# Performance work log

Hardware: AMD Instinct MI355X
Metric: run time of the kernel (lower is better)

## Reference

```python
import jax, jax.numpy as jnp
import numpy as np

TOP_K = 4
TAU = 1.0  # training-mode temperature
EPS_NORM = 1e-12
EPS_G = 1e-10


def l2_normalize(x, axis=-1):
    sq = jnp.sum(x * x, axis=axis, keepdims=True)
    return x * jax.lax.rsqrt(jnp.maximum(sq, EPS_NORM))


def setup_inputs() -> dict:
    key = jax.random.key(0)
    k1, k2, k3, k4 = jax.random.split(key, 4)
    B, S, D = 256, 196, 1024
    P, L = 512, 8
    x_embed = jax.random.normal(k1, (B, S, D), dtype=jnp.float32)
    prompt = jax.random.normal(k2, (P, L, D), dtype=jnp.float32) * 0.02
    prompt_key = jax.random.normal(k3, (P, D), dtype=jnp.float32) * 0.02
    gumbel_u = jax.random.uniform(k4, (TOP_K, B, P), dtype=jnp.float32)
    return {"x_embed": x_embed, "prompt": prompt, "prompt_key": prompt_key,
            "gumbel_u": gumbel_u}


def reference(x_embed, prompt, prompt_key, gumbel_u):
    # query: mean over sequence dim (embedding_key='mean')  -> [B, D]
    query = jnp.mean(x_embed, axis=1)
    key_n = l2_normalize(prompt_key, axis=1)   # [P, D]
    q_n = l2_normalize(query, axis=1)          # [B, D]
    sim = jnp.matmul(q_n, key_n.T)             # [B, P]

    P = prompt.shape[0]
    cur = sim
    selected = []
    for i in range(TOP_K):
        # Gumbel(0,1) noise from uniform samples
        g = -jnp.log(-jnp.log(gumbel_u[i] + EPS_G) + EPS_G)
        soft = jax.nn.softmax((cur + g) / TAU, axis=-1)      # [B, P]
        hard = jax.nn.one_hot(jnp.argmax(soft, axis=-1), P, dtype=soft.dtype)
        w = soft + jax.lax.stop_gradient(hard - soft)        # straight-through
        # weighted combination over pool -> [B, L, D]
        sel = jnp.einsum('bp,pld->bld', w, prompt)
        selected.append(sel)
        # training-mode mask-out of selected entries
        cur = cur - w * 1000.0
    return jnp.concatenate(selected, axis=1)  # [B, TOP_K*L, D]
```

## Files before the change

kernel.cpp:

```cpp
#include <hip/hip_runtime.h>
#include <hip/hip_bf16.h>
#include <math.h>

#define B   256
#define S   196
#define D   1024
#define P   512
#define L   8
#define TOPK 4

#define SSPLIT 7
#define SCHUNK (S / SSPLIT)
#define KSPLIT 8

__global__ __launch_bounds__(256) void mean_partial_kernel(
    const float* __restrict__ x, float* __restrict__ part) {
  const int b = blockIdx.x;
  const int j = blockIdx.y;
  const int t = threadIdx.x;
  const float* xb = x + (size_t)b * S * D + (size_t)j * SCHUNK * D + t * 4;

  float4 acc = make_float4(0.f, 0.f, 0.f, 0.f);
#pragma unroll 4
  for (int s = 0; s < SCHUNK; ++s) {
    float4 v = *(const float4*)(xb + (size_t)s * D);
    acc.x += v.x; acc.y += v.y; acc.z += v.z; acc.w += v.w;
  }
  *(float4*)(part + ((size_t)b * SSPLIT + j) * D + t * 4) = acc;
}

__global__ __launch_bounds__(256) void norm_kernel(
    const float* __restrict__ part, const float* __restrict__ pk,
    float* __restrict__ qn, float* __restrict__ kn) {
  const int t = threadIdx.x;
  float4 acc;
  float* dst;

  if (blockIdx.x < B) {
    const int b = blockIdx.x;
    acc = make_float4(0.f, 0.f, 0.f, 0.f);
#pragma unroll
    for (int j = 0; j < SSPLIT; ++j) {
      float4 v = *(const float4*)(part + ((size_t)b * SSPLIT + j) * D + t * 4);
      acc.x += v.x; acc.y += v.y; acc.z += v.z; acc.w += v.w;
    }
    const float inv = 1.0f / (float)S;
    acc.x *= inv; acc.y *= inv; acc.z *= inv; acc.w *= inv;
    dst = qn + (size_t)b * D + t * 4;
  } else {
    const int p = blockIdx.x - B;
    acc = *(const float4*)(pk + (size_t)p * D + t * 4);
    dst = kn + (size_t)p * D + t * 4;
  }

  float ss = acc.x * acc.x + acc.y * acc.y + acc.z * acc.z + acc.w * acc.w;
  for (int off = 32; off > 0; off >>= 1) ss += __shfl_down(ss, off, 64);
  __shared__ float wsum[4];
  __shared__ float snorm;
  const int lane = t & 63, w = t >> 6;
  if (lane == 0) wsum[w] = ss;
  __syncthreads();
  if (t == 0) {
    float tot = wsum[0] + wsum[1] + wsum[2] + wsum[3];
    snorm = rsqrtf(fmaxf(tot, 1e-12f));
  }
  __syncthreads();
  const float r = snorm;
  *(float4*)dst = make_float4(acc.x * r, acc.y * r, acc.z * r, acc.w * r);
}

#define KK 16
__global__ __launch_bounds__(256) void sim_kernel(
    const float* __restrict__ qn, const float* __restrict__ kn,
    float* __restrict__ simp) {
  const int b0 = blockIdx.x * 64;
  const int p0 = blockIdx.y * 64;
  const int z  = blockIdx.z;
  const int k0 = z * (D / KSPLIT);
  const int t = threadIdx.x;
  const int tx = t & 15;
  const int ty = t >> 4;

  __shared__ float As[KK][68];
  __shared__ float Bs[KK][68];

  float acc[4][4];
#pragma unroll
  for (int i = 0; i < 4; ++i)
#pragma unroll
    for (int j = 0; j < 4; ++j) acc[i][j] = 0.f;

  const int rr = t >> 2;
  const int k4 = (t & 3) * 4;

  for (int kt = 0; kt < D / KSPLIT; kt += KK) {
    float4 a = *(const float4*)(qn + (size_t)(b0 + rr) * D + k0 + kt + k4);
    float4 bb = *(const float4*)(kn + (size_t)(p0 + rr) * D + k0 + kt + k4);
    As[k4 + 0][rr] = a.x; As[k4 + 1][rr] = a.y;
    As[k4 + 2][rr] = a.z; As[k4 + 3][rr] = a.w;
    Bs[k4 + 0][rr] = bb.x; Bs[k4 + 1][rr] = bb.y;
    Bs[k4 + 2][rr] = bb.z; Bs[k4 + 3][rr] = bb.w;
    __syncthreads();
#pragma unroll
    for (int kk = 0; kk < KK; ++kk) {
      float4 av = *(const float4*)&As[kk][ty * 4];
      float4 bv = *(const float4*)&Bs[kk][tx * 4];
      acc[0][0] += av.x * bv.x; acc[0][1] += av.x * bv.y;
      acc[0][2] += av.x * bv.z; acc[0][3] += av.x * bv.w;
      acc[1][0] += av.y * bv.x; acc[1][1] += av.y * bv.y;
      acc[1][2] += av.y * bv.z; acc[1][3] += av.y * bv.w;
      acc[2][0] += av.z * bv.x; acc[2][1] += av.z * bv.y;
      acc[2][2] += av.z * bv.z; acc[2][3] += av.z * bv.w;
      acc[3][0] += av.w * bv.x; acc[3][1] += av.w * bv.y;
      acc[3][2] += av.w * bv.z; acc[3][3] += av.w * bv.w;
    }
    __syncthreads();
  }
#pragma unroll
  for (int i = 0; i < 4; ++i)
#pragma unroll
    for (int j = 0; j < 4; ++j)
      simp[((size_t)z * B + b0 + ty * 4 + i) * P + p0 + tx * 4 + j] =
          acc[i][j];
}

__global__ __launch_bounds__(256) void select_gather_kernel(
    const float* __restrict__ simp, const float* __restrict__ gu,
    const float* __restrict__ prompt, float* __restrict__ out) {
  const int b = blockIdx.x;
  const int t = threadIdx.x;
  __shared__ float cur[P];

  float c0 = 0.f, c1 = 0.f;
#pragma unroll
  for (int z = 0; z < KSPLIT; ++z) {
    c0 += simp[((size_t)z * B + b) * P + t];
    c1 += simp[((size_t)z * B + b) * P + t + 256];
  }
  cur[t] = c0;
  cur[t + 256] = c1;
  __syncthreads();

  __shared__ float wval[4];
  __shared__ int widx[4];
  __shared__ int sidx[TOPK];

  for (int i = 0; i < TOPK; ++i) {
    const float* gui = gu + ((size_t)i * B + b) * P;
    float u0 = gui[t];
    float u1 = gui[t + 256];
    float g0 = -logf(-logf(u0 + 1e-10f) + 1e-10f);
    float g1 = -logf(-logf(u1 + 1e-10f) + 1e-10f);
    float v0 = cur[t] + g0;
    float v1 = cur[t + 256] + g1;
    float bv = v0; int bi = t;
    if (v1 > bv) { bv = v1; bi = t + 256; }
    for (int off = 32; off > 0; off >>= 1) {
      float ov = __shfl_down(bv, off, 64);
      int oi = __shfl_down(bi, off, 64);
      if (ov > bv || (ov == bv && oi < bi)) { bv = ov; bi = oi; }
    }
    const int lane = t & 63, w = t >> 6;
    if (lane == 0) { wval[w] = bv; widx[w] = bi; }
    __syncthreads();
    if (t == 0) {
      float bestv = wval[0]; int besti = widx[0];
      for (int k = 1; k < 4; ++k)
        if (wval[k] > bestv || (wval[k] == bestv && widx[k] < besti)) {
          bestv = wval[k]; besti = widx[k];
        }
      sidx[i] = besti;
      cur[besti] -= 1000.0f;
    }
    __syncthreads();
  }

#pragma unroll
  for (int i = 0; i < TOPK; ++i) {
    const int p = sidx[i];
    const float4* src = (const float4*)(prompt + (size_t)p * L * D);
    float4* dst = (float4*)(out + ((size_t)b * (TOPK * L) + i * L) * D);
#pragma unroll
    for (int l = 0; l < L; ++l) {
      dst[l * (D / 4) + t] = src[l * (D / 4) + t];
    }
  }
}

extern "C" void kernel_launch(void* const* d_in, const int* in_sizes, int n_in,
                              void* d_out, int out_size, void* d_ws,
                              size_t ws_size, hipStream_t stream) {
  const float* x_embed    = (const float*)d_in[0];
  const float* prompt     = (const float*)d_in[1];
  const float* prompt_key = (const float*)d_in[2];
  const float* gumbel_u   = (const float*)d_in[3];
  float* out = (float*)d_out;

  float* simp = (float*)d_ws;
  float* qn   = simp + (size_t)KSPLIT * B * P;
  float* kn   = qn + (size_t)B * D;
  float* part = kn + (size_t)P * D;

  mean_partial_kernel<<<dim3(B, SSPLIT), 256, 0, stream>>>(x_embed, part);
  norm_kernel<<<B + P, 256, 0, stream>>>(part, prompt_key, qn, kn);
  sim_kernel<<<dim3(B / 64, P / 64, KSPLIT), 256, 0, stream>>>(qn, kn, simp);
  select_gather_kernel<<<B, 256, 0, stream>>>(simp, gumbel_u, prompt, out);
}
```

Measured before the change: 329.8 us.

## Fuse normalization, similarity and selection into one kernel using output as scratch

Removes the separate norm and split-K similarity GEMM kernels. Each batch block now computes its query mean and norm, then dots the query against all prompt keys while computing key norms on the fly, then does the Gumbel top-k selection and gather. Partial means are stored in the output buffer as scratch instead of a workspace. This cuts two launches and the intermediate global traffic, but every block redundantly rereads the full prompt_key matrix and recomputes key norms.

```diff
diff --git a/kernel.cpp b/kernel.cpp
--- a/kernel.cpp
+++ b/kernel.cpp
@@ -1,20 +1,19 @@
 #include <hip/hip_runtime.h>
-#include <hip/hip_bf16.h>
 #include <math.h>
 
-#define B   256
-#define S   196
-#define D   1024
-#define P   512
-#define L   8
+#define B    256
+#define S    196
+#define D    1024
+#define P    512
+#define L    8
 #define TOPK 4
 
 #define SSPLIT 7
 #define SCHUNK (S / SSPLIT)
-#define KSPLIT 8
+#define OUTSTRIDE (TOPK * L * D)
 
 __global__ __launch_bounds__(256) void mean_partial_kernel(
-    const float* __restrict__ x, float* __restrict__ part) {
+    const float* __restrict__ x, float* __restrict__ scratch) {
   const int b = blockIdx.x;
   const int j = blockIdx.y;
   const int t = threadIdx.x;
@@ -26,151 +25,99 @@
     float4 v = *(const float4*)(xb + (size_t)s * D);
     acc.x += v.x; acc.y += v.y; acc.z += v.z; acc.w += v.w;
   }
-  *(float4*)(part + ((size_t)b * SSPLIT + j) * D + t * 4) = acc;
+  *(float4*)(scratch + (size_t)b * OUTSTRIDE + j * D + t * 4) = acc;
 }
 
-__global__ __launch_bounds__(256) void norm_kernel(
-    const float* __restrict__ part, const float* __restrict__ pk,
-    float* __restrict__ qn, float* __restrict__ kn) {
-  const int t = threadIdx.x;
-  float4 acc;
-  float* dst;
-
-  if (blockIdx.x < B) {
-    const int b = blockIdx.x;
-    acc = make_float4(0.f, 0.f, 0.f, 0.f);
-#pragma unroll
-    for (int j = 0; j < SSPLIT; ++j) {
-      float4 v = *(const float4*)(part + ((size_t)b * SSPLIT + j) * D + t * 4);
-      acc.x += v.x; acc.y += v.y; acc.z += v.z; acc.w += v.w;
-    }
-    const float inv = 1.0f / (float)S;
-    acc.x *= inv; acc.y *= inv; acc.z *= inv; acc.w *= inv;
-    dst = qn + (size_t)b * D + t * 4;
-  } else {
-    const int p = blockIdx.x - B;
-    acc = *(const float4*)(pk + (size_t)p * D + t * 4);
-    dst = kn + (size_t)p * D + t * 4;
-  }
-
-  float ss = acc.x * acc.x + acc.y * acc.y + acc.z * acc.z + acc.w * acc.w;
-  for (int off = 32; off > 0; off >>= 1) ss += __shfl_down(ss, off, 64);
-  __shared__ float wsum[4];
-  __shared__ float snorm;
-  const int lane = t & 63, w = t >> 6;
-  if (lane == 0) wsum[w] = ss;
-  __syncthreads();
-  if (t == 0) {
-    float tot = wsum[0] + wsum[1] + wsum[2] + wsum[3];
-    snorm = rsqrtf(fmaxf(tot, 1e-12f));
-  }
-  __syncthreads();
-  const float r = snorm;
-  *(float4*)dst = make_float4(acc.x * r, acc.y * r, acc.z * r, acc.w * r);
-}
-
-#define KK 16
-__global__ __launch_bounds__(256) void sim_kernel(
-    const float* __restrict__ qn, const float* __restrict__ kn,
-    float* __restrict__ simp) {
-  const int b0 = blockIdx.x * 64;
-  const int p0 = blockIdx.y * 64;
-  const int z  = blockIdx.z;
-  const int k0 = z * (D / KSPLIT);
-  const int t = threadIdx.x;
-  const int tx = t & 15;
-  const int ty = t >> 4;
-
-  __shared__ float As[KK][68];
-  __shared__ float Bs[KK][68];
-
-  float acc[4][4];
-#pragma unroll
-  for (int i = 0; i < 4; ++i)
-#pragma unroll
-    for (int j = 0; j < 4; ++j) acc[i][j] = 0.f;
-
-  const int rr = t >> 2;
-  const int k4 = (t & 3) * 4;
-
-  for (int kt = 0; kt < D / KSPLIT; kt += KK) {
-    float4 a = *(const float4*)(qn + (size_t)(b0 + rr) * D + k0 + kt + k4);
-    float4 bb = *(const float4*)(kn + (size_t)(p0 + rr) * D + k0 + kt + k4);
-    As[k4 + 0][rr] = a.x; As[k4 + 1][rr] = a.y;
-    As[k4 + 2][rr] = a.z; As[k4 + 3][rr] = a.w;
-    Bs[k4 + 0][rr] = bb.x; Bs[k4 + 1][rr] = bb.y;
-    Bs[k4 + 2][rr] = bb.z; Bs[k4 + 3][rr] = bb.w;
-    __syncthreads();
-#pragma unroll
-    for (int kk = 0; kk < KK; ++kk) {
-      float4 av = *(const float4*)&As[kk][ty * 4];
-      float4 bv = *(const float4*)&Bs[kk][tx * 4];
-      acc[0][0] += av.x * bv.x; acc[0][1] += av.x * bv.y;
-      acc[0][2] += av.x * bv.z; acc[0][3] += av.x * bv.w;
-      acc[1][0] += av.y * bv.x; acc[1][1] += av.y * bv.y;
-      acc[1][2] += av.y * bv.z; acc[1][3] += av.y * bv.w;
-      acc[2][0] += av.z * bv.x; acc[2][1] += av.z * bv.y;
-      acc[2][2] += av.z * bv.z; acc[2][3] += av.z * bv.w;
-      acc[3][0] += av.w * bv.x; acc[3][1] += av.w * bv.y;
-      acc[3][2] += av.w * bv.z; acc[3][3] += av.w * bv.w;
-    }
-    __syncthreads();
-  }
-#pragma unroll
-  for (int i = 0; i < 4; ++i)
-#pragma unroll
-    for (int j = 0; j < 4; ++j)
-      simp[((size_t)z * B + b0 + ty * 4 + i) * P + p0 + tx * 4 + j] =
-          acc[i][j];
-}
-
-__global__ __launch_bounds__(256) void select_gather_kernel(
-    const float* __restrict__ simp, const float* __restrict__ gu,
+__global__ __launch_bounds__(512) void fused_select_kernel(
+    const float* __restrict__ pk, const float* __restrict__ gu,
     const float* __restrict__ prompt, float* __restrict__ out) {
   const int b = blockIdx.x;
   const int t = threadIdx.x;
+  const int lane = t & 63;
+  const int wv = t >> 6;
+
+  __shared__ float q[D];
   __shared__ float cur[P];
+  __shared__ float wred[8];
+  __shared__ int   wids[8];
+  __shared__ float s_rq;
+  __shared__ int   sidx[TOPK];
 
-  float c0 = 0.f, c1 = 0.f;
+  if (t < 256) {
+    const float* part = out + (size_t)b * OUTSTRIDE;
+    float4 m4 = make_float4(0.f, 0.f, 0.f, 0.f);
 #pragma unroll
-  for (int z = 0; z < KSPLIT; ++z) {
-    c0 += simp[((size_t)z * B + b) * P + t];
-    c1 += simp[((size_t)z * B + b) * P + t + 256];
+    for (int j = 0; j < SSPLIT; ++j) {
+      float4 v = *(const float4*)(part + j * D + t * 4);
+      m4.x += v.x; m4.y += v.y; m4.z += v.z; m4.w += v.w;
+    }
+    const float inv = 1.0f / (float)S;
+    m4.x *= inv; m4.y *= inv; m4.z *= inv; m4.w *= inv;
+    *(float4*)(q + t * 4) = m4;
+    float ss = m4.x * m4.x + m4.y * m4.y + m4.z * m4.z + m4.w * m4.w;
+    for (int off = 32; off > 0; off >>= 1) ss += __shfl_down(ss, off, 64);
+    if (lane == 0) wred[wv] = ss;
   }
-  cur[t] = c0;
-  cur[t + 256] = c1;
+  __syncthreads();
+  if (t == 0) {
+    float tot = wred[0] + wred[1] + wred[2] + wred[3];
+    s_rq = rsqrtf(fmaxf(tot, 1e-12f));
+  }
+  __syncthreads();
+  const float rq = s_rq;
+
+  {
+    const int pbase = wv * 64;
+    for (int r = 0; r < 64; r += 2) {
+      const float* k0 = pk + (size_t)(pbase + r) * D;
+      const float* k1 = pk + (size_t)(pbase + r + 1) * D;
+      float s1a = 0.f, s2a = 0.f, s1b = 0.f, s2b = 0.f;
+#pragma unroll
+      for (int kk = 0; kk < 4; ++kk) {
+        const int di = lane * 4 + kk * 256;
+        float4 qv = *(const float4*)(q + di);
+        float4 ka = *(const float4*)(k0 + di);
+        float4 kb = *(const float4*)(k1 + di);
+        s1a += qv.x * ka.x + qv.y * ka.y + qv.z * ka.z + qv.w * ka.w;
+        s2a += ka.x * ka.x + ka.y * ka.y + ka.z * ka.z + ka.w * ka.w;
+        s1b += qv.x * kb.x + qv.y * kb.y + qv.z * kb.z + qv.w * kb.w;
+        s2b += kb.x * kb.x + kb.y * kb.y + kb.z * kb.z + kb.w * kb.w;
+      }
+      for (int off = 32; off > 0; off >>= 1) {
+        s1a += __shfl_down(s1a, off, 64);
+        s2a += __shfl_down(s2a, off, 64);
+        s1b += __shfl_down(s1b, off, 64);
+        s2b += __shfl_down(s2b, off, 64);
+      }
+      if (lane == 0) {
+        cur[pbase + r]     = s1a * rsqrtf(fmaxf(s2a, 1e-12f)) * rq;
+        cur[pbase + r + 1] = s1b * rsqrtf(fmaxf(s2b, 1e-12f)) * rq;
+      }
+    }
+  }
   __syncthreads();
 
-  __shared__ float wval[4];
-  __shared__ int widx[4];
-  __shared__ int sidx[TOPK];
-
   for (int i = 0; i < TOPK; ++i) {
-    const float* gui = gu + ((size_t)i * B + b) * P;
-    float u0 = gui[t];
-    float u1 = gui[t + 256];
-    float g0 = -logf(-logf(u0 + 1e-10f) + 1e-10f);
-    float g1 = -logf(-logf(u1 + 1e-10f) + 1e-10f);
-    float v0 = cur[t] + g0;
-    float v1 = cur[t + 256] + g1;
-    float bv = v0; int bi = t;
-    if (v1 > bv) { bv = v1; bi = t + 256; }
+    const float u = gu[((size_t)i * B + b) * P + t];
+    const float g = -logf(-logf(u + 1e-10f) + 1e-10f);
+    float v = cur[t] + g;
+    int idx = t;
     for (int off = 32; off > 0; off >>= 1) {
-      float ov = __shfl_down(bv, off, 64);
-      int oi = __shfl_down(bi, off, 64);
-      if (ov > bv || (ov == bv && oi < bi)) { bv = ov; bi = oi; }
+      float ov = __shfl_down(v, off, 64);
+      int oi = __shfl_down(idx, off, 64);
+      if (ov > v || (ov == v && oi < idx)) { v = ov; idx = oi; }
     }
-    const int lane = t & 63, w = t >> 6;
-    if (lane == 0) { wval[w] = bv; widx[w] = bi; }
+    if (lane == 0) { wred[wv] = v; wids[wv] = idx; }
     __syncthreads();
     if (t == 0) {
-      float bestv = wval[0]; int besti = widx[0];
-      for (int k = 1; k < 4; ++k)
-        if (wval[k] > bestv || (wval[k] == bestv && widx[k] < besti)) {
-          bestv = wval[k]; besti = widx[k];
+      float bv = wred[0]; int bi = wids[0];
+#pragma unroll
+      for (int k = 1; k < 8; ++k)
+        if (wred[k] > bv || (wred[k] == bv && wids[k] < bi)) {
+          bv = wred[k]; bi = wids[k];
         }
-      sidx[i] = besti;
-      cur[besti] -= 1000.0f;
+      sidx[i] = bi;
+      cur[bi] -= 1000.0f;
     }
     __syncthreads();
   }
@@ -179,10 +126,10 @@
   for (int i = 0; i < TOPK; ++i) {
     const int p = sidx[i];
     const float4* src = (const float4*)(prompt + (size_t)p * L * D);
-    float4* dst = (float4*)(out + ((size_t)b * (TOPK * L) + i * L) * D);
+    float4* dst = (float4*)(out + (size_t)b * OUTSTRIDE + i * (L * D));
 #pragma unroll
-    for (int l = 0; l < L; ++l) {
-      dst[l * (D / 4) + t] = src[l * (D / 4) + t];
+    for (int c = 0; c < (L * D / 4) / 512; ++c) {
+      dst[c * 512 + t] = src[c * 512 + t];
     }
   }
 }
@@ -196,13 +143,7 @@
   const float* gumbel_u   = (const float*)d_in[3];
   float* out = (float*)d_out;
 
-  float* simp = (float*)d_ws;
-  float* qn   = simp + (size_t)KSPLIT * B * P;
-  float* kn   = qn + (size_t)B * D;
-  float* part = kn + (size_t)P * D;
-
-  mean_partial_kernel<<<dim3(B, SSPLIT), 256, 0, stream>>>(x_embed, part);
-  norm_kernel<<<B + P, 256, 0, stream>>>(part, prompt_key, qn, kn);
-  sim_kernel<<<dim3(B / 64, P / 64, KSPLIT), 256, 0, stream>>>(qn, kn, simp);
-  select_gather_kernel<<<B, 256, 0, stream>>>(simp, gumbel_u, prompt, out);
+  mean_partial_kernel<<<dim3(B, SSPLIT), 256, 0, stream>>>(x_embed, out);
+  fused_select_kernel<<<B, 512, 0, stream>>>(prompt_key, gumbel_u, prompt,
+                                             out);
 }
```

Result: slower. 358.9 us (+8.8%).

## Split select and gather into separate kernels for wider gather parallelism

Applied to the files above, without the earlier changes.

The fused select+gather kernel is split in two. The select kernel now uses 512 threads, one per pool entry, precomputes all Gumbel noise up front, and keeps each score in a register. A separate gather kernel copies the selected prompt rows using B*TOPK*2 blocks instead of B, which spreads the 32 MB output write across many more workgroups. The cost is an extra kernel launch plus a small global round-trip for the indices.

```diff
diff --git a/kernel.cpp b/kernel.cpp
--- a/kernel.cpp
+++ b/kernel.cpp
@@ -1,12 +1,11 @@
 #include <hip/hip_runtime.h>
-#include <hip/hip_bf16.h>
 #include <math.h>
 
-#define B   256
-#define S   196
-#define D   1024
-#define P   512
-#define L   8
+#define B    256
+#define S    196
+#define D    1024
+#define P    512
+#define L    8
 #define TOPK 4
 
 #define SSPLIT 7
@@ -124,67 +123,67 @@
           acc[i][j];
 }
 
-__global__ __launch_bounds__(256) void select_gather_kernel(
+__global__ __launch_bounds__(512) void select_kernel(
     const float* __restrict__ simp, const float* __restrict__ gu,
-    const float* __restrict__ prompt, float* __restrict__ out) {
+    int* __restrict__ sidx) {
   const int b = blockIdx.x;
   const int t = threadIdx.x;
-  __shared__ float cur[P];
-
-  float c0 = 0.f, c1 = 0.f;
-#pragma unroll
-  for (int z = 0; z < KSPLIT; ++z) {
-    c0 += simp[((size_t)z * B + b) * P + t];
-    c1 += simp[((size_t)z * B + b) * P + t + 256];
-  }
-  cur[t] = c0;
-  cur[t + 256] = c1;
-  __syncthreads();
-
-  __shared__ float wval[4];
-  __shared__ int widx[4];
-  __shared__ int sidx[TOPK];
-
+  const int lane = t & 63, wv = t >> 6;
+
+  float c = 0.f;
+#pragma unroll
+  for (int z = 0; z < KSPLIT; ++z)
+    c += simp[((size_t)z * B + b) * P + t];
+
+  float g[TOPK];
+#pragma unroll
   for (int i = 0; i < TOPK; ++i) {
-    const float* gui = gu + ((size_t)i * B + b) * P;
-    float u0 = gui[t];
-    float u1 = gui[t + 256];
-    float g0 = -logf(-logf(u0 + 1e-10f) + 1e-10f);
-    float g1 = -logf(-logf(u1 + 1e-10f) + 1e-10f);
-    float v0 = cur[t] + g0;
-    float v1 = cur[t + 256] + g1;
-    float bv = v0; int bi = t;
-    if (v1 > bv) { bv = v1; bi = t + 256; }
+    float u = gu[((size_t)i * B + b) * P + t];
+    g[i] = -logf(-logf(u + 1e-10f) + 1e-10f);
+  }
+
+  __shared__ float wval[8];
+  __shared__ int   widx[8];
+  __shared__ int   ssel[TOPK];
+
+  for (int i = 0; i < TOPK; ++i) {
+    float v = c + g[i];
+    int idx = t;
     for (int off = 32; off > 0; off >>= 1) {
-      float ov = __shfl_down(bv, off, 64);
-      int oi = __shfl_down(bi, off, 64);
-      if (ov > bv || (ov == bv && oi < bi)) { bv = ov; bi = oi; }
-    }
-    const int lane = t & 63, w = t >> 6;
-    if (lane == 0) { wval[w] = bv; widx[w] = bi; }
+      float ov = __shfl_down(v, off, 64);
+      int oi = __shfl_down(idx, off, 64);
+      if (ov > v || (ov == v && oi < idx)) { v = ov; idx = oi; }
+    }
+    if (lane == 0) { wval[wv] = v; widx[wv] = idx; }
     __syncthreads();
     if (t == 0) {
-      float bestv = wval[0]; int besti = widx[0];
-      for (int k = 1; k < 4; ++k)
-        if (wval[k] > bestv || (wval[k] == bestv && widx[k] < besti)) {
-          bestv = wval[k]; besti = widx[k];
+      float bv = wval[0]; int bi = widx[0];
+#pragma unroll
+      for (int k = 1; k < 8; ++k)
+        if (wval[k] > bv || (wval[k] == bv && widx[k] < bi)) {
+          bv = wval[k]; bi = widx[k];
         }
-      sidx[i] = besti;
-      cur[besti] -= 1000.0f;
-    }
-    __syncthreads();
-  }
-
-#pragma unroll
-  for (int i = 0; i < TOPK; ++i) {
-    const int p = sidx[i];
-    const float4* src = (const float4*)(prompt + (size_t)p * L * D);
-    float4* dst = (float4*)(out + ((size_t)b * (TOPK * L) + i * L) * D);
-#pragma unroll
-    for (int l = 0; l < L; ++l) {
-      dst[l * (D / 4) + t] = src[l * (D / 4) + t];
-    }
-  }
+      ssel[i] = bi;
+    }
+    __syncthreads();
+    if (t == ssel[i]) c -= 1000.0f;
+  }
+  if (t < TOPK) sidx[b * TOPK + t] = ssel[t];
+}
+
+__global__ __launch_bounds__(256) void gather_kernel(
+    const int* __restrict__ sidx, const float* __restrict__ prompt,
+    float* __restrict__ out) {
+  const int bi = blockIdx.x;
+  const int h = blockIdx.y;
+  const int t = threadIdx.x;
+  const int p = sidx[bi];
+  const float4* src =
+      (const float4*)(prompt + (size_t)p * L * D) + h * 1024;
+  float4* dst = (float4*)(out + (size_t)bi * (L * D)) + h * 1024;
+#pragma unroll
+  for (int c = 0; c < 4; ++c)
+    dst[c * 256 + t] = src[c * 256 + t];
 }
 
 extern "C" void kernel_launch(void* const* d_in, const int* in_sizes, int n_in,
@@ -200,9 +199,11 @@
   float* qn   = simp + (size_t)KSPLIT * B * P;
   float* kn   = qn + (size_t)B * D;
   float* part = kn + (size_t)P * D;
+  int*   sidx = (int*)(part + (size_t)B * SSPLIT * D);
 
   mean_partial_kernel<<<dim3(B, SSPLIT), 256, 0, stream>>>(x_embed, part);
   norm_kernel<<<B + P, 256, 0, stream>>>(part, prompt_key, qn, kn);
   sim_kernel<<<dim3(B / 64, P / 64, KSPLIT), 256, 0, stream>>>(qn, kn, simp);
-  select_gather_kernel<<<B, 256, 0, stream>>>(simp, gumbel_u, prompt, out);
-}
+  select_kernel<<<B, 512, 0, stream>>>(simp, gumbel_u, sidx);
+  gather_kernel<<<dim3(B * TOPK, 2), 256, 0, stream>>>(sidx, prompt, out);
+}
```

Result: no change. 332.0 us (+0.7%).
